# Performance work log

Hardware: AMD Instinct MI355X
Metric: run time of the kernel (lower is better)

The kernel has to match this reference:

```python
import jax, jax.numpy as jnp
import numpy as np

NEG_SLOPE = 0.2   # PyG GATConv default negative_slope
NUM_GRAPHS = 64   # graphs per batched timestep (max batch id + 1)


def setup_inputs() -> dict:
    key = jax.random.key(0)
    ks = jax.random.split(key, 16)
    T, N, E, F, H, C, B = 8, 20000, 320000, 128, 128, 16, NUM_GRAPHS
    x = jax.random.normal(ks[0], (T, N, F), dtype=jnp.float32)
    edge_index = jax.random.randint(ks[1], (T, 2, E), 0, N, dtype=jnp.int32)
    batch = jnp.sort(jax.random.randint(ks[2], (N,), 0, B, dtype=jnp.int32))
    z = jax.random.normal(ks[3], (B, H), dtype=jnp.float32)
    s_f = 1.0 / np.sqrt(F)
    s_h = 1.0 / np.sqrt(H)
    return {
        "x": x, "edge_index": edge_index, "batch": batch, "z": z,
        "gat_W": jax.random.normal(ks[4], (F, H), jnp.float32) * s_f,
        "att_src": jax.random.normal(ks[5], (H,), jnp.float32) * s_h,
        "att_dst": jax.random.normal(ks[6], (H,), jnp.float32) * s_h,
        "gat_bias": jnp.zeros((H,), jnp.float32),
        "W_ih": jax.random.normal(ks[7], (4 * H, H), jnp.float32) * s_h,
        "W_hh": jax.random.normal(ks[8], (4 * H, H), jnp.float32) * s_h,
        "b_ih": jnp.zeros((4 * H,), jnp.float32),
        "b_hh": jnp.zeros((4 * H,), jnp.float32),
        "fc_W": jax.random.normal(ks[9], (C, 2 * H), jnp.float32) * (1.0 / np.sqrt(2 * H)),
        "fc_b": jnp.zeros((C,), jnp.float32),
    }


def _gat_conv(x, edge_index, W, a_src, a_dst, bias):
    # PyG GATConv, heads=1, add_self_loops=True: gather -> softmax-per-target -> scatter
    N = x.shape[0]
    h = x @ W                                        # [N, H]
    loops = jnp.arange(N, dtype=edge_index.dtype)
    src = jnp.concatenate([edge_index[0], loops])    # message source j
    dst = jnp.concatenate([edge_index[1], loops])    # message target i
    e = jax.nn.leaky_relu((h @ a_src)[src] + (h @ a_dst)[dst], NEG_SLOPE)  # [E+N]
    m = jax.ops.segment_max(e, dst, num_segments=N)  # stable softmax over incoming edges
    w = jnp.exp(e - m[dst])
    denom = jax.ops.segment_sum(w, dst, num_segments=N)
    alpha = w / denom[dst]
    out = jax.ops.segment_sum(alpha[:, None] * h[src], dst, num_segments=N)
    return out + bias


def reference(x, edge_index, batch, z, gat_W, att_src, att_dst, gat_bias,
              W_ih, W_hh, b_ih, b_hh, fc_W, fc_b):
    B = NUM_GRAPHS
    # per-timestep GAT (vmapped over the window) + global mean pool
    node_feats = jax.vmap(lambda xt, ei: _gat_conv(xt, ei, gat_W, att_src, att_dst, gat_bias))(x, edge_index)  # [T,N,H]
    counts = jnp.maximum(jax.ops.segment_sum(jnp.ones_like(batch, jnp.float32), batch, num_segments=B), 1.0)
    pooled = jax.vmap(lambda f: jax.ops.segment_sum(f, batch, num_segments=B))(node_feats) / counts[None, :, None]  # [T,B,H]

    # LSTM over T (PyTorch gate order i, f, g, o)
    H = gat_W.shape[1]
    h0 = jnp.zeros((B, H), x.dtype)

    def step(carry, xt):
        h, c = carry
        gates = xt @ W_ih.T + b_ih + h @ W_hh.T + b_hh
        i, f, g, o = jnp.split(gates, 4, axis=-1)
        c = jax.nn.sigmoid(f) * c + jax.nn.sigmoid(i) * jnp.tanh(g)
        h = jax.nn.sigmoid(o) * jnp.tanh(c)
        return (h, c), None

    (h_n, _), _ = jax.lax.scan(step, (h0, h0), pooled)
    # dropout is identity at inference
    return jnp.concatenate([h_n, z], axis=1) @ fc_W.T + fc_b  # [B, num_classes]
```

## Files before the change

### kernel.cpp

```cpp
#include <hip/hip_runtime.h>
#include <math.h>

#define TT 8
#define NNODES 20000
#define NEDGES 320000
#define FDIM 128
#define HDIM 128
#define BGR 64
#define NCLS 16
#define NB 157
#define CB 80
#define EC 4000
#define CAP 2816
#define CLSC 133

__device__ __forceinline__ float lrelu(float x) { return fmaxf(x, 0.2f * x); }
__device__ __forceinline__ float sigmoidf(float x) { return 1.0f / (1.0f + __expf(-x)); }
__device__ __forceinline__ float tanh_fast(float x) {
  return 1.0f - 2.0f / (__expf(2.0f * x) + 1.0f);
}
__device__ __forceinline__ unsigned short f2bf(float f) {
  unsigned int u = __float_as_uint(f);
  unsigned int r = (u + 0x7fff + ((u >> 16) & 1)) >> 16;
  return (unsigned short)r;
}
__device__ __forceinline__ float bf_lo(unsigned int u) { return __uint_as_float(u << 16); }
__device__ __forceinline__ float bf_hi(unsigned int u) { return __uint_as_float(u & 0xffff0000u); }

__global__ __launch_bounds__(256) void k_prep(
    const float* __restrict__ W, const float* __restrict__ att_s, const float* __restrict__ att_d,
    float* __restrict__ u, float* __restrict__ v) {
  const int tid = threadIdx.x;
  if (tid < 128) {
    float su = 0.f, sv = 0.f;
    const float4* wr = (const float4*)(W + (size_t)tid * 128);
    #pragma unroll 8
    for (int q = 0; q < 32; ++q) {
      float4 w4 = wr[q];
      float4 a4 = *(const float4*)(att_s + q * 4);
      float4 d4 = *(const float4*)(att_d + q * 4);
      su += w4.x * a4.x + w4.y * a4.y + w4.z * a4.z + w4.w * a4.w;
      sv += w4.x * d4.x + w4.y * d4.y + w4.z * d4.z + w4.w * d4.w;
    }
    u[tid] = su; v[tid] = sv;
  }
}

__global__ __launch_bounds__(256) void k_gemv(
    const float* __restrict__ x, const float* __restrict__ u, const float* __restrict__ v,
    float* __restrict__ as_, float* __restrict__ ad_, float* __restrict__ denom) {
  const int tid = threadIdx.x;
  const int c4 = tid & 31;
  const int ty = tid >> 5;
  const int lane = tid & 63;
  float4 uu = *(const float4*)(u + c4 * 4);
  float4 vv = *(const float4*)(v + c4 * 4);
  const int base = blockIdx.x * 64;
  #pragma unroll
  for (int it = 0; it < 8; ++it) {
    int r = base + it * 8 + ty;
    float4 xv = *(const float4*)(x + (size_t)r * FDIM + c4 * 4);
    float ps = xv.x * uu.x + xv.y * uu.y + xv.z * uu.z + xv.w * uu.w;
    float pd = xv.x * vv.x + xv.y * vv.y + xv.z * vv.z + xv.w * vv.w;
    #pragma unroll
    for (int o = 16; o > 0; o >>= 1) { ps += __shfl_xor(ps, o); pd += __shfl_xor(pd, o); }
    if ((lane & 31) == 0) {
      as_[r] = ps;
      ad_[r] = pd;
      denom[r] = __expf(lrelu(ps + pd));
    }
  }
}

__global__ __launch_bounds__(256) void k_scat(
    const int* __restrict__ ei, int* __restrict__ cnt_d, int* __restrict__ cnt_s,
    unsigned int* __restrict__ part_d, unsigned int* __restrict__ part_s) {
  __shared__ unsigned int buf[EC];
  __shared__ int hd[NB], hs[NB];
  __shared__ int bd[NB], bs[NB];
  const int tid = threadIdx.x;
  const int chunk = blockIdx.x, t = blockIdx.y;
  if (tid < NB) { hd[tid] = 0; hs[tid] = 0; }
  __syncthreads();
  const int* eis = ei + (size_t)t * 2 * NEDGES;
  for (int i = tid; i < EC; i += 256) {
    int e = chunk * EC + i;
    int s = eis[e], d = eis[NEDGES + e];
    buf[i] = ((unsigned int)s << 15) | (unsigned int)d;
    atomicAdd(&hd[d >> 7], 1);
    atomicAdd(&hs[s >> 7], 1);
  }
  __syncthreads();
  if (tid < NB) {
    bd[tid] = atomicAdd(&cnt_d[t * NB + tid], hd[tid]);
    bs[tid] = atomicAdd(&cnt_s[t * NB + tid], hs[tid]);
    hd[tid] = 0; hs[tid] = 0;
  }
  __syncthreads();
  unsigned int* pdt = part_d + (size_t)t * NB * CAP;
  unsigned int* pst = part_s + (size_t)t * NB * CAP;
  for (int i = tid; i < EC; i += 256) {
    unsigned int rec = buf[i];
    int d = rec & 32767, s = rec >> 15;
    int Bd = d >> 7, Bs = s >> 7;
    int od = bd[Bd] + atomicAdd(&hd[Bd], 1);
    pdt[Bd * CAP + od] = rec;
    int os = bs[Bs] + atomicAdd(&hs[Bs], 1);
    pst[Bs * CAP + os] = rec;
  }
}

__global__ __launch_bounds__(256) void k_denomB(
    const unsigned int* __restrict__ part_d, const int* __restrict__ cnt_d,
    const float* __restrict__ as_, const float* __restrict__ ad_,
    const float* __restrict__ dseed, const int* __restrict__ batch,
    float4* __restrict__ aux4, int* __restrict__ starts) {
  __shared__ float hist[128];
  __shared__ float adl[128];
  const int tid = threadIdx.x;
  const int B = blockIdx.x, t = blockIdx.y;
  if (tid < 128) {
    hist[tid] = 0.f;
    int n = B * 128 + tid;
    adl[tid] = (n < NNODES) ? ad_[t * NNODES + n] : 0.f;
  }
  __syncthreads();
  const int cnt = cnt_d[t * NB + B];
  const unsigned int* pdt = part_d + ((size_t)t * NB + B) * CAP;
  const float* asb = as_ + (size_t)t * NNODES;
  for (int i = tid; i < cnt; i += 256) {
    unsigned int rec = pdt[i];
    int d = rec & 32767, s = rec >> 15;
    float w = __expf(lrelu(asb[s] + adl[d & 127]));
    atomicAdd(&hist[d & 127], w);
  }
  __syncthreads();
  if (tid < 128) {
    int n = B * 128 + tid;
    if (n < NNODES) {
      float den = dseed[t * NNODES + n] + hist[tid];
      int bn = batch[n];
      aux4[t * NNODES + n] = make_float4(adl[tid], 1.0f / den, __int_as_float(bn), 0.f);
      if (t == 0) {
        if (n == 0) { for (int bb = 0; bb <= bn; ++bb) starts[bb] = 0; }
        else { int pb = batch[n - 1]; for (int bb = pb + 1; bb <= bn; ++bb) starts[bb] = n; }
        if (n == NNODES - 1) { for (int bb = bn + 1; bb <= BGR; ++bb) starts[bb] = NNODES; }
      }
    }
  }
}

__global__ __launch_bounds__(256) void k_cpgemm(
    const unsigned int* __restrict__ part_s, const int* __restrict__ cnt_s,
    const float* __restrict__ as_, const float4* __restrict__ aux4,
    const float* __restrict__ x, float* __restrict__ ppart) {
  __shared__ float cl[BGR * CLSC];
  __shared__ float asl[128];
  const int tid = threadIdx.x;
  const int B = blockIdx.x, t = blockIdx.y;
  #pragma unroll
  for (int i = tid; i < BGR * CLSC; i += 256) cl[i] = 0.f;
  if (tid < 128) {
    int n = B * 128 + tid;
    asl[tid] = (n < NNODES) ? as_[t * NNODES + n] : 0.f;
  }
  __syncthreads();
  const float4* auxt = aux4 + (size_t)t * NNODES;
  if (tid < 128) {
    int n = B * 128 + tid;
    if (n < NNODES) {
      float4 a2 = auxt[n];
      float wself = __expf(lrelu(asl[tid] + a2.x)) * a2.y;
      cl[__float_as_int(a2.z) * CLSC + tid] = wself;
    }
  }
  {
    const int cnt = cnt_s[t * NB + B];
    const unsigned int* pst = part_s + ((size_t)t * NB + B) * CAP;
    int i = tid;
    for (; i + 768 < cnt; i += 1024) {
      unsigned int r0 = pst[i], r1 = pst[i + 256], r2 = pst[i + 512], r3 = pst[i + 768];
      float4 a0 = auxt[r0 & 32767], a1 = auxt[r1 & 32767];
      float4 a2 = auxt[r2 & 32767], a3 = auxt[r3 & 32767];
      float w0 = __expf(lrelu(asl[r0 >> 15 & 127] + a0.x)) * a0.y;
      float w1 = __expf(lrelu(asl[r1 >> 15 & 127] + a1.x)) * a1.y;
      float w2 = __expf(lrelu(asl[r2 >> 15 & 127] + a2.x)) * a2.y;
      float w3 = __expf(lrelu(asl[r3 >> 15 & 127] + a3.x)) * a3.y;
      atomicAdd(&cl[__float_as_int(a0.z) * CLSC + (int)(r0 >> 15 & 127)], w0);
      atomicAdd(&cl[__float_as_int(a1.z) * CLSC + (int)(r1 >> 15 & 127)], w1);
      atomicAdd(&cl[__float_as_int(a2.z) * CLSC + (int)(r2 >> 15 & 127)], w2);
      atomicAdd(&cl[__float_as_int(a3.z) * CLSC + (int)(r3 >> 15 & 127)], w3);
    }
    for (; i < cnt; i += 256) {
      unsigned int rec = pst[i];
      int s7 = (int)(rec >> 15) & 127;
      float4 aa = auxt[rec & 32767];
      float w = __expf(lrelu(asl[s7] + aa.x)) * aa.y;
      atomicAdd(&cl[__float_as_int(aa.z) * CLSC + s7], w);
    }
  }
  __syncthreads();
  const int bq = tid >> 4;
  const int dq = tid & 15;
  const float* xbase = x + (size_t)t * NNODES * FDIM;
  float acc[4][8] = {};
  #pragma unroll 4
  for (int kk = 0; kk < 128; ++kk) {
    int row = B * 128 + kk;
    row = (row < NNODES) ? row : (NNODES - 1);
    const float* xr = xbase + (size_t)row * FDIM;
    float xd[8];
    *(float4*)&xd[0] = *(const float4*)(xr + dq * 4);
    *(float4*)&xd[4] = *(const float4*)(xr + 64 + dq * 4);
    float cv[4];
    #pragma unroll
    for (int i = 0; i < 4; ++i) cv[i] = cl[(bq * 4 + i) * CLSC + kk];
    #pragma unroll
    for (int i = 0; i < 4; ++i)
      #pragma unroll
      for (int d = 0; d < 8; ++d)
        acc[i][d] += cv[i] * xd[d];
  }
  float* pp = ppart + ((size_t)t * NB + B) * BGR * HDIM;
  #pragma unroll
  for (int i = 0; i < 4; ++i) {
    *(float4*)(pp + (bq * 4 + i) * HDIM + dq * 4)      = make_float4(acc[i][0], acc[i][1], acc[i][2], acc[i][3]);
    *(float4*)(pp + (bq * 4 + i) * HDIM + 64 + dq * 4) = make_float4(acc[i][4], acc[i][5], acc[i][6], acc[i][7]);
  }
}

__global__ __launch_bounds__(128) void k_pw(
    const float* __restrict__ ppart, const int* __restrict__ starts,
    const float* __restrict__ W, const float* __restrict__ gat_bias,
    float* __restrict__ pooled) {
  __shared__ float srow[128];
  const int tb = blockIdx.x;
  const int t = tb >> 6, b = tb & 63;
  const int d = threadIdx.x;
  float s = 0.f;
  const float* pp = ppart + ((size_t)t * NB * BGR + b) * HDIM + d;
  #pragma unroll 4
  for (int B = 0; B < NB; ++B) s += pp[(size_t)B * BGR * HDIM];
  srow[d] = s;
  __syncthreads();
  const float invc = 1.0f / (float)max(starts[b + 1] - starts[b], 1);
  float o = 0.f;
  #pragma unroll 8
  for (int k = 0; k < 128; ++k) o += srow[k] * W[k * 128 + d];
  pooled[(size_t)(t * BGR + b) * HDIM + d] = o * invc + gat_bias[d];
}

__global__ __launch_bounds__(512) void k_lstm_fc(
    const float* __restrict__ pooled,
    const float* __restrict__ W_ih, const float* __restrict__ W_hh,
    const float* __restrict__ b_ih, const float* __restrict__ b_hh,
    const float* __restrict__ z, const float* __restrict__ fc_W,
    const float* __restrict__ fc_b, float* __restrict__ out) {
  const int b = blockIdx.x;
  const int g = threadIdx.x;
  __shared__ unsigned int wpk[512 * 65];
  __shared__ float hv[128], cv[128], part[512];
  __shared__ float pool8[TT][128];
  __shared__ float fcp[16][17];

  #pragma unroll 2
  for (int it = 0; it < 64; ++it) {
    int i = g + it * 512;
    int gr = i >> 6, j = i & 63;
    float2 wv = *(const float2*)(W_hh + (size_t)gr * HDIM + j * 2);
    wpk[gr * 65 + j] = (unsigned int)f2bf(wv.x) | ((unsigned int)f2bf(wv.y) << 16);
  }
  #pragma unroll
  for (int i = 0; i < 2; ++i) {
    int idx = g + i * 512;
    int t = idx >> 7, k = idx & 127;
    pool8[t][k] = pooled[((size_t)t * BGR + b) * HDIM + k];
  }
  if (g < 128) { hv[g] = 0.f; cv[g] = 0.f; }
  __syncthreads();

  float gx[8] = {};
  {
    const float4* wi = (const float4*)(W_ih + (size_t)g * HDIM);
    #pragma unroll 2
    for (int k4 = 0; k4 < 32; ++k4) {
      float4 wv = wi[k4];
      #pragma unroll
      for (int t = 0; t < TT; ++t) {
        float4 p = *(const float4*)(&pool8[t][k4 * 4]);
        gx[t] += wv.x * p.x + wv.y * p.y + wv.z * p.z + wv.w * p.w;
      }
    }
  }
  const float bsum = b_ih[g] + b_hh[g];
  const unsigned int* wr = &wpk[g * 65];
  const float4* hv4 = (const float4*)hv;
  #pragma unroll
  for (int t = 0; t < TT; ++t) {
    float s = gx[t] + bsum;
    #pragma unroll 8
    for (int j2 = 0; j2 < 32; ++j2) {
      unsigned int w0 = wr[2 * j2], w1 = wr[2 * j2 + 1];
      float4 hh = hv4[j2];
      s += bf_lo(w0) * hh.x + bf_hi(w0) * hh.y + bf_lo(w1) * hh.z + bf_hi(w1) * hh.w;
    }
    part[g] = s;
    __syncthreads();
    if (g < 128) {
      float ig = sigmoidf(part[g]);
      float fg = sigmoidf(part[128 + g]);
      float gc = tanh_fast(part[256 + g]);
      float og = sigmoidf(part[384 + g]);
      float c = fg * cv[g] + ig * gc;
      cv[g] = c;
      hv[g] = og * tanh_fast(c);
    }
    __syncthreads();
  }
  if (g < 256) {
    const int c = g >> 4, kp = g & 15;
    float s = 0.f;
    for (int k = kp * 16; k < kp * 16 + 16; ++k) {
      float v = (k < 128) ? hv[k] : z[(size_t)b * HDIM + (k - 128)];
      s += v * fc_W[(size_t)c * 256 + k];
    }
    fcp[c][kp] = s;
  }
  __syncthreads();
  if (g < 16) {
    float r = fc_b[g];
    #pragma unroll
    for (int k = 0; k < 16; ++k) r += fcp[g][k];
    out[(size_t)b * NCLS + g] = r;
  }
}

extern "C" void kernel_launch(void* const* d_in, const int* in_sizes, int n_in,
                              void* d_out, int out_size, void* d_ws, size_t ws_size,
                              hipStream_t stream) {
  const float* x       = (const float*)d_in[0];
  const int*   ei      = (const int*)d_in[1];
  const int*   batch   = (const int*)d_in[2];
  const float* z       = (const float*)d_in[3];
  const float* gat_W   = (const float*)d_in[4];
  const float* att_src = (const float*)d_in[5];
  const float* att_dst = (const float*)d_in[6];
  const float* gat_bias= (const float*)d_in[7];
  const float* W_ih    = (const float*)d_in[8];
  const float* W_hh    = (const float*)d_in[9];
  const float* b_ih    = (const float*)d_in[10];
  const float* b_hh    = (const float*)d_in[11];
  const float* fc_W    = (const float*)d_in[12];
  const float* fc_b    = (const float*)d_in[13];
  float* out = (float*)d_out;

  char* ws = (char*)d_ws;
  size_t off = 0;
  auto alloc = [&](size_t bytes) {
    void* p = (void*)(ws + off);
    off += (bytes + 255) & ~(size_t)255;
    return p;
  };
  float*  as_    = (float*)alloc((size_t)TT * NNODES * 4);
  float*  ad_    = (float*)alloc((size_t)TT * NNODES * 4);
  float*  denom  = (float*)alloc((size_t)TT * NNODES * 4);
  float4* aux4   = (float4*)alloc((size_t)TT * NNODES * 16);
  int*    cnt2   = (int*)alloc((size_t)2 * TT * NB * 4);
  int*    cnt_d  = cnt2;
  int*    cnt_s  = cnt2 + TT * NB;
  unsigned int* part_d = (unsigned int*)alloc(((size_t)TT * NB + 1) * CAP * 4);
  unsigned int* part_s = (unsigned int*)alloc(((size_t)TT * NB + 1) * CAP * 4);
  float* ppart = (float*)alloc((size_t)TT * NB * BGR * HDIM * 4);
  float* uvec  = (float*)alloc(128 * 4);
  float* vvec  = (float*)alloc(128 * 4);
  float* pooled = (float*)alloc((size_t)TT * BGR * HDIM * 4);
  int* starts = (int*)alloc((BGR + 1) * 4);
  (void)ws_size; (void)in_sizes; (void)n_in; (void)out_size;

  hipMemsetAsync(cnt2, 0, (size_t)2 * TT * NB * 4, stream);

  k_prep<<<1, 256, 0, stream>>>(gat_W, att_src, att_dst, uvec, vvec);
  k_gemv<<<(TT * NNODES) / 64, 256, 0, stream>>>(x, uvec, vvec, as_, ad_, denom);
  k_scat<<<dim3(CB, TT), 256, 0, stream>>>(ei, cnt_d, cnt_s, part_d, part_s);
  k_denomB<<<dim3(NB, TT), 256, 0, stream>>>(part_d, cnt_d, as_, ad_, denom, batch, aux4, starts);
  k_cpgemm<<<dim3(NB, TT), 256, 0, stream>>>(part_s, cnt_s, as_, aux4, x, ppart);
  k_pw<<<TT * BGR, 128, 0, stream>>>(ppart, starts, gat_W, gat_bias, pooled);
  k_lstm_fc<<<BGR, 512, 0, stream>>>(pooled, W_ih, W_hh, b_ih, b_hh, z, fc_W, fc_b, out);
}
```

Measured before the change: 200.5 us.

## Store x and partial pooled sums in bf16, transpose coefficient tile, unroll denom loop

The gemv kernel now also writes a packed bf16 copy of x, which the per-block GEMM reads in place of fp32 x, halving its global traffic. The partial pooled results are stored as packed bf16, so the reduction kernel reads half as many bytes. The shared coefficient matrix is transposed so the GEMM reads a float4 per step, with source attention values taken by wave shuffles instead of from shared memory. The denominator histogram loop is unrolled four-way to overlap its gathers. This trades an extra bf16 write pass over x, plus bf16 rounding of inputs and partials, against fewer bytes read in the main kernels.

Measured after the change: 202.7 us. About the same (+1.1%).

```diff
diff --git a/kernel.cpp b/kernel.cpp
--- a/kernel.cpp
+++ b/kernel.cpp
@@ -12,7 +12,6 @@
 #define CB 80
 #define EC 4000
 #define CAP 2816
-#define CLSC 133
 
 __device__ __forceinline__ float lrelu(float x) { return fmaxf(x, 0.2f * x); }
 __device__ __forceinline__ float sigmoidf(float x) { return 1.0f / (1.0f + __expf(-x)); }
@@ -48,7 +47,8 @@
 
 __global__ __launch_bounds__(256) void k_gemv(
     const float* __restrict__ x, const float* __restrict__ u, const float* __restrict__ v,
-    float* __restrict__ as_, float* __restrict__ ad_, float* __restrict__ denom) {
+    float* __restrict__ as_, float* __restrict__ ad_, float* __restrict__ denom,
+    unsigned int* __restrict__ xb) {
   const int tid = threadIdx.x;
   const int c4 = tid & 31;
   const int ty = tid >> 5;
@@ -62,6 +62,19 @@
     float4 xv = *(const float4*)(x + (size_t)r * FDIM + c4 * 4);
     float ps = xv.x * uu.x + xv.y * uu.y + xv.z * uu.z + xv.w * uu.w;
     float pd = xv.x * vv.x + xv.y * vv.y + xv.z * vv.z + xv.w * vv.w;
+    float4 px;
+    px.x = __shfl_xor(xv.x, 16);
+    px.y = __shfl_xor(xv.y, 16);
+    px.z = __shfl_xor(xv.z, 16);
+    px.w = __shfl_xor(xv.w, 16);
+    if (c4 < 16) {
+      uint4 pk;
+      pk.x = (unsigned int)f2bf(xv.x) | ((unsigned int)f2bf(px.x) << 16);
+      pk.y = (unsigned int)f2bf(xv.y) | ((unsigned int)f2bf(px.y) << 16);
+      pk.z = (unsigned int)f2bf(xv.z) | ((unsigned int)f2bf(px.z) << 16);
+      pk.w = (unsigned int)f2bf(xv.w) | ((unsigned int)f2bf(px.w) << 16);
+      *(uint4*)(xb + (size_t)r * 64 + c4 * 4) = pk;
+    }
     #pragma unroll
     for (int o = 16; o > 0; o >>= 1) { ps += __shfl_xor(ps, o); pd += __shfl_xor(pd, o); }
     if ((lane & 31) == 0) {
@@ -128,11 +141,23 @@
   const int cnt = cnt_d[t * NB + B];
   const unsigned int* pdt = part_d + ((size_t)t * NB + B) * CAP;
   const float* asb = as_ + (size_t)t * NNODES;
-  for (int i = tid; i < cnt; i += 256) {
+  int i = tid;
+  for (; i + 768 < cnt; i += 1024) {
+    unsigned int r0 = pdt[i], r1 = pdt[i + 256], r2 = pdt[i + 512], r3 = pdt[i + 768];
+    float v0 = asb[r0 >> 15], v1 = asb[r1 >> 15], v2 = asb[r2 >> 15], v3 = asb[r3 >> 15];
+    float w0 = __expf(lrelu(v0 + adl[r0 & 127]));
+    float w1 = __expf(lrelu(v1 + adl[r1 & 127]));
+    float w2 = __expf(lrelu(v2 + adl[r2 & 127]));
+    float w3 = __expf(lrelu(v3 + adl[r3 & 127]));
+    atomicAdd(&hist[r0 & 127], w0);
+    atomicAdd(&hist[r1 & 127], w1);
+    atomicAdd(&hist[r2 & 127], w2);
+    atomicAdd(&hist[r3 & 127], w3);
+  }
+  for (; i < cnt; i += 256) {
     unsigned int rec = pdt[i];
-    int d = rec & 32767, s = rec >> 15;
-    float w = __expf(lrelu(asb[s] + adl[d & 127]));
-    atomicAdd(&hist[d & 127], w);
+    float w = __expf(lrelu(asb[rec >> 15] + adl[rec & 127]));
+    atomicAdd(&hist[rec & 127], w);
   }
   __syncthreads();
   if (tid < 128) {
@@ -153,25 +178,24 @@
 __global__ __launch_bounds__(256) void k_cpgemm(
     const unsigned int* __restrict__ part_s, const int* __restrict__ cnt_s,
     const float* __restrict__ as_, const float4* __restrict__ aux4,
-    const float* __restrict__ x, float* __restrict__ ppart) {
-  __shared__ float cl[BGR * CLSC];
-  __shared__ float asl[128];
+    const unsigned int* __restrict__ xb, unsigned int* __restrict__ ppart) {
+  __shared__ float clT[128 * 64];
   const int tid = threadIdx.x;
+  const int lane = tid & 63;
   const int B = blockIdx.x, t = blockIdx.y;
   #pragma unroll
-  for (int i = tid; i < BGR * CLSC; i += 256) cl[i] = 0.f;
-  if (tid < 128) {
-    int n = B * 128 + tid;
-    asl[tid] = (n < NNODES) ? as_[t * NNODES + n] : 0.f;
-  }
+  for (int i = tid; i < 128 * 64; i += 256) clT[i] = 0.f;
+  const float* asb = as_ + (size_t)t * NNODES;
+  float a0 = asb[min(B * 128 + lane, NNODES - 1)];
+  float a1 = asb[min(B * 128 + 64 + lane, NNODES - 1)];
   __syncthreads();
   const float4* auxt = aux4 + (size_t)t * NNODES;
   if (tid < 128) {
     int n = B * 128 + tid;
     if (n < NNODES) {
-      float4 a2 = auxt[n];
-      float wself = __expf(lrelu(asl[tid] + a2.x)) * a2.y;
-      cl[__float_as_int(a2.z) * CLSC + tid] = wself;
+      float4 aa = auxt[n];
+      float wself = __expf(lrelu(asb[n] + aa.x)) * aa.y;
+      atomicAdd(&clT[tid * 64 + __float_as_int(aa.z)], wself);
     }
   }
   {
@@ -180,68 +204,88 @@
     int i = tid;
     for (; i + 768 < cnt; i += 1024) {
       unsigned int r0 = pst[i], r1 = pst[i + 256], r2 = pst[i + 512], r3 = pst[i + 768];
-      float4 a0 = auxt[r0 & 32767], a1 = auxt[r1 & 32767];
-      float4 a2 = auxt[r2 & 32767], a3 = auxt[r3 & 32767];
-      float w0 = __expf(lrelu(asl[r0 >> 15 & 127] + a0.x)) * a0.y;
-      float w1 = __expf(lrelu(asl[r1 >> 15 & 127] + a1.x)) * a1.y;
-      float w2 = __expf(lrelu(asl[r2 >> 15 & 127] + a2.x)) * a2.y;
-      float w3 = __expf(lrelu(asl[r3 >> 15 & 127] + a3.x)) * a3.y;
-      atomicAdd(&cl[__float_as_int(a0.z) * CLSC + (int)(r0 >> 15 & 127)], w0);
-      atomicAdd(&cl[__float_as_int(a1.z) * CLSC + (int)(r1 >> 15 & 127)], w1);
-      atomicAdd(&cl[__float_as_int(a2.z) * CLSC + (int)(r2 >> 15 & 127)], w2);
-      atomicAdd(&cl[__float_as_int(a3.z) * CLSC + (int)(r3 >> 15 & 127)], w3);
+      float4 x0 = auxt[r0 & 32767], x1 = auxt[r1 & 32767];
+      float4 x2 = auxt[r2 & 32767], x3 = auxt[r3 & 32767];
+      int s0 = (int)(r0 >> 15) & 127, s1 = (int)(r1 >> 15) & 127;
+      int s2 = (int)(r2 >> 15) & 127, s3 = (int)(r3 >> 15) & 127;
+      float p0 = __shfl(a0, s0 & 63), q0 = __shfl(a1, s0 & 63);
+      float p1 = __shfl(a0, s1 & 63), q1 = __shfl(a1, s1 & 63);
+      float p2 = __shfl(a0, s2 & 63), q2 = __shfl(a1, s2 & 63);
+      float p3 = __shfl(a0, s3 & 63), q3 = __shfl(a1, s3 & 63);
+      float v0 = (s0 & 64) ? q0 : p0, v1 = (s1 & 64) ? q1 : p1;
+      float v2 = (s2 & 64) ? q2 : p2, v3 = (s3 & 64) ? q3 : p3;
+      float w0 = __expf(lrelu(v0 + x0.x)) * x0.y;
+      float w1 = __expf(lrelu(v1 + x1.x)) * x1.y;
+      float w2 = __expf(lrelu(v2 + x2.x)) * x2.y;
+      float w3 = __expf(lrelu(v3 + x3.x)) * x3.y;
+      atomicAdd(&clT[s0 * 64 + __float_as_int(x0.z)], w0);
+      atomicAdd(&clT[s1 * 64 + __float_as_int(x1.z)], w1);
+      atomicAdd(&clT[s2 * 64 + __float_as_int(x2.z)], w2);
+      atomicAdd(&clT[s3 * 64 + __float_as_int(x3.z)], w3);
     }
     for (; i < cnt; i += 256) {
       unsigned int rec = pst[i];
       int s7 = (int)(rec >> 15) & 127;
       float4 aa = auxt[rec & 32767];
-      float w = __expf(lrelu(asl[s7] + aa.x)) * aa.y;
-      atomicAdd(&cl[__float_as_int(aa.z) * CLSC + s7], w);
+      float p = __shfl(a0, s7 & 63), q = __shfl(a1, s7 & 63);
+      float v = (s7 & 64) ? q : p;
+      float w = __expf(lrelu(v + aa.x)) * aa.y;
+      atomicAdd(&clT[s7 * 64 + __float_as_int(aa.z)], w);
     }
   }
   __syncthreads();
   const int bq = tid >> 4;
   const int dq = tid & 15;
-  const float* xbase = x + (size_t)t * NNODES * FDIM;
+  const unsigned int* xrow = xb + (size_t)t * NNODES * 64;
   float acc[4][8] = {};
   #pragma unroll 4
   for (int kk = 0; kk < 128; ++kk) {
     int row = B * 128 + kk;
     row = (row < NNODES) ? row : (NNODES - 1);
-    const float* xr = xbase + (size_t)row * FDIM;
+    uint4 u4 = *(const uint4*)(xrow + (size_t)row * 64 + dq * 4);
     float xd[8];
-    *(float4*)&xd[0] = *(const float4*)(xr + dq * 4);
-    *(float4*)&xd[4] = *(const float4*)(xr + 64 + dq * 4);
+    xd[0] = bf_lo(u4.x); xd[4] = bf_hi(u4.x);
+    xd[1] = bf_lo(u4.y); xd[5] = bf_hi(u4.y);
+    xd[2] = bf_lo(u4.z); xd[6] = bf_hi(u4.z);
+    xd[3] = bf_lo(u4.w); xd[7] = bf_hi(u4.w);
     float cv[4];
-    #pragma unroll
-    for (int i = 0; i < 4; ++i) cv[i] = cl[(bq * 4 + i) * CLSC + kk];
+    *(float4*)cv = *(const float4*)&clT[kk * 64 + bq * 4];
     #pragma unroll
     for (int i = 0; i < 4; ++i)
       #pragma unroll
       for (int d = 0; d < 8; ++d)
         acc[i][d] += cv[i] * xd[d];
   }
-  float* pp = ppart + ((size_t)t * NB + B) * BGR * HDIM;
+  unsigned int* pp = ppart + ((size_t)t * NB + B) * BGR * 64;
   #pragma unroll
   for (int i = 0; i < 4; ++i) {
-    *(float4*)(pp + (bq * 4 + i) * HDIM + dq * 4)      = make_float4(acc[i][0], acc[i][1], acc[i][2], acc[i][3]);
-    *(float4*)(pp + (bq * 4 + i) * HDIM + 64 + dq * 4) = make_float4(acc[i][4], acc[i][5], acc[i][6], acc[i][7]);
+    uint4 pk;
+    pk.x = (unsigned int)f2bf(acc[i][0]) | ((unsigned int)f2bf(acc[i][4]) << 16);
+    pk.y = (unsigned int)f2bf(acc[i][1]) | ((unsigned int)f2bf(acc[i][5]) << 16);
+    pk.z = (unsigned int)f2bf(acc[i][2]) | ((unsigned int)f2bf(acc[i][6]) << 16);
+    pk.w = (unsigned int)f2bf(acc[i][3]) | ((unsigned int)f2bf(acc[i][7]) << 16);
+    *(uint4*)(pp + (bq * 4 + i) * 64 + dq * 4) = pk;
   }
 }
 
 __global__ __launch_bounds__(128) void k_pw(
-    const float* __restrict__ ppart, const int* __restrict__ starts,
+    const unsigned int* __restrict__ ppart, const int* __restrict__ starts,
     const float* __restrict__ W, const float* __restrict__ gat_bias,
     float* __restrict__ pooled) {
   __shared__ float srow[128];
   const int tb = blockIdx.x;
   const int t = tb >> 6, b = tb & 63;
   const int d = threadIdx.x;
-  float s = 0.f;
-  const float* pp = ppart + ((size_t)t * NB * BGR + b) * HDIM + d;
-  #pragma unroll 4
-  for (int B = 0; B < NB; ++B) s += pp[(size_t)B * BGR * HDIM];
-  srow[d] = s;
+  if (d < 64) {
+    float slo = 0.f, shi = 0.f;
+    const unsigned int* pp = ppart + ((size_t)t * NB * BGR + b) * 64 + d;
+    #pragma unroll 4
+    for (int B = 0; B < NB; ++B) {
+      unsigned int u = pp[(size_t)B * BGR * 64];
+      slo += bf_lo(u); shi += bf_hi(u);
+    }
+    srow[d] = slo; srow[64 + d] = shi;
+  }
   __syncthreads();
   const float invc = 1.0f / (float)max(starts[b + 1] - starts[b], 1);
   float o = 0.f;
@@ -370,7 +414,8 @@
   int*    cnt_s  = cnt2 + TT * NB;
   unsigned int* part_d = (unsigned int*)alloc(((size_t)TT * NB + 1) * CAP * 4);
   unsigned int* part_s = (unsigned int*)alloc(((size_t)TT * NB + 1) * CAP * 4);
-  float* ppart = (float*)alloc((size_t)TT * NB * BGR * HDIM * 4);
+  unsigned int* ppart  = (unsigned int*)alloc((size_t)TT * NB * BGR * 64 * 4);
+  unsigned int* xb     = (unsigned int*)alloc((size_t)TT * NNODES * 64 * 4);
   float* uvec  = (float*)alloc(128 * 4);
   float* vvec  = (float*)alloc(128 * 4);
   float* pooled = (float*)alloc((size_t)TT * BGR * HDIM * 4);
@@ -380,10 +425,10 @@
   hipMemsetAsync(cnt2, 0, (size_t)2 * TT * NB * 4, stream);
 
   k_prep<<<1, 256, 0, stream>>>(gat_W, att_src, att_dst, uvec, vvec);
-  k_gemv<<<(TT * NNODES) / 64, 256, 0, stream>>>(x, uvec, vvec, as_, ad_, denom);
+  k_gemv<<<(TT * NNODES) / 64, 256, 0, stream>>>(x, uvec, vvec, as_, ad_, denom, xb);
   k_scat<<<dim3(CB, TT), 256, 0, stream>>>(ei, cnt_d, cnt_s, part_d, part_s);
   k_denomB<<<dim3(NB, TT), 256, 0, stream>>>(part_d, cnt_d, as_, ad_, denom, batch, aux4, starts);
-  k_cpgemm<<<dim3(NB, TT), 256, 0, stream>>>(part_s, cnt_s, as_, aux4, x, ppart);
+  k_cpgemm<<<dim3(NB, TT), 256, 0, stream>>>(part_s, cnt_s, as_, aux4, xb, ppart);
   k_pw<<<TT * BGR, 128, 0, stream>>>(ppart, starts, gat_W, gat_bias, pooled);
   k_lstm_fc<<<BGR, 512, 0, stream>>>(pooled, W_ih, W_hh, b_ih, b_hh, z, fc_W, fc_b, out);
 }
```
